# Kernel tuning notes

Hardware: AMD Instinct MI355X
Metric: run time of the kernel (lower is better)

Reference implementation:

```python
import jax, jax.numpy as jnp
import numpy as np
import math

D = 2048  # hidden_size
B, S = 4, 2048
EPS = 1e-5


def _ln(z, g, b):
    m = jnp.mean(z, axis=-1, keepdims=True)
    v = jnp.mean(jnp.square(z - m), axis=-1, keepdims=True)
    return (z - m) * jax.lax.rsqrt(v + EPS) * g + b


def _rotate_half(x):
    h = x.shape[-1] // 2
    return jnp.concatenate([-x[..., h:], x[..., :h]], axis=-1)


def _mas_normalize(logits):
    m = jnp.max(jnp.abs(logits), axis=-1, keepdims=True)
    return logits / (m + 1e-9)


def setup_inputs() -> dict:
    key = jax.random.key(0)
    ks = jax.random.split(key, 12)
    std = 0.02
    return {
        "x": jax.random.normal(ks[0], (B, S, D), dtype=jnp.float32),
        "position_ids": jnp.arange(S, dtype=jnp.int32),
        "ln1_g": jnp.ones((D,), jnp.float32),
        "ln1_b": jnp.zeros((D,), jnp.float32),
        # stacked params for [q, k, v, o]
        "mu_w": std * jax.random.normal(ks[1], (4, D, D), dtype=jnp.float32),
        "mu_b": jnp.zeros((4, D), jnp.float32),
        "proto_w": std * jax.random.normal(ks[2], (4, D, D), dtype=jnp.float32),
        "gate": jnp.zeros((4, D), jnp.float32),
        "pt_w": std * jax.random.normal(ks[3], (4, D, D), dtype=jnp.float32),
        "pln_g": jnp.ones((4, D), jnp.float32),
        "pln_b": jnp.zeros((4, D), jnp.float32),
        "incoming": std * jax.random.normal(ks[4], (4, D, D), dtype=jnp.float32),
    }


def reference(x, position_ids, ln1_g, ln1_b, mu_w, mu_b, proto_w, gate,
              pt_w, pln_g, pln_b, incoming):
    d = x.shape[-1]
    inv_sqrt_d = 1.0 / math.sqrt(d)

    # proto_state = proto_weight + LN(Linear(incoming))  per module [4, D, D]
    prc = jnp.einsum('nij,noj->nio', incoming, pt_w)
    proto_state = proto_w + _ln(prc, pln_g[:, None, :], pln_b[:, None, :])

    ln1_out = _ln(x, ln1_g, ln1_b)            # [B,S,D]
    ctx = jnp.mean(ln1_out, axis=1)           # [B,D]

    # qkv computation outputs: silu(ln1_out @ mu_w.T + mu_b) for n in {q,k,v}
    comp = jax.nn.silu(jnp.einsum('bsd,nod->nbso', ln1_out, mu_w[:3])
                       + mu_b[:3][:, None, None, :])            # [3,B,S,D]
    # routing from context vector
    match_ctx = jnp.einsum('bd,nod->nbo', ctx, proto_state[:3]) * inv_sqrt_d
    routing = match_ctx + gate[:3][:, None, :]                  # [3,B,D]
    gating = _mas_normalize(routing)
    masked = gating[:, :, None, :] * comp                       # [3,B,S,D]
    q, k, v = masked[0], masked[1], masked[2]

    # RoPE over full hidden dim (num_heads == 1)
    seq = position_ids.shape[0]
    inv_freq = 1.0 / (10000.0 ** (jnp.arange(0, d, 2, dtype=jnp.float32) / d))
    t = jnp.arange(seq, dtype=jnp.float32)
    freqs = t[:, None] * inv_freq[None, :]
    emb = jnp.concatenate([freqs, freqs], axis=-1)              # [S,D]
    cos = jnp.cos(emb)[position_ids]
    sin = jnp.sin(emb)[position_ids]
    q = q * cos + _rotate_half(q) * sin
    k = k * cos + _rotate_half(k) * sin

    # causal single-head attention, scale 1/sqrt(head_dim=D)
    scores = jnp.einsum('bqd,bkd->bqk', q, k) * inv_sqrt_d      # [B,S,S]
    causal = jnp.tril(jnp.ones((seq, seq), dtype=bool))
    scores = jnp.where(causal, scores, jnp.finfo(scores.dtype).min)
    probs = jax.nn.softmax(scores, axis=-1)
    attn_out = jnp.einsum('bqk,bkd->bqd', probs, v)             # [B,S,D]

    # output SPL + routing
    ctx_o = jnp.mean(attn_out, axis=1)
    c_o = jax.nn.silu(jnp.einsum('bsd,od->bso', attn_out, mu_w[3]) + mu_b[3])
    match_o = jnp.einsum('bd,od->bo', ctx_o, proto_state[3]) * inv_sqrt_d
    gating_o = _mas_normalize(match_o + gate[3])
    x_out = x + gating_o[:, None, :] * c_o
    return x_out
```

## Files before the change

### kernel.cpp

```cpp
#include <hip/hip_runtime.h>
#include <hip/hip_bf16.h>
#include <hip/hip_fp16.h>

#define Dh 2048
#define Bh 4
#define Sh 2048
#define NROW 8192
#define HALF 1024
#define INV_SQRT_D 0.022097086912079608f
#define LNEPS 1e-5f

typedef __hip_bfloat16 bf16;
typedef short short8 __attribute__((ext_vector_type(8)));
typedef float f32x4 __attribute__((ext_vector_type(4)));
typedef unsigned short ushort8v __attribute__((ext_vector_type(8)));
typedef unsigned short ushort4v __attribute__((ext_vector_type(4)));

__device__ inline float h2f_bits(unsigned short u) {
  __half h;
  *(unsigned short*)&h = u;
  return __half2float(h);
}

__device__ inline float warp_sum(float x) {
#pragma unroll
  for (int o = 32; o > 0; o >>= 1) x += __shfl_down(x, o);
  return x;
}
__device__ inline float warp_max(float x) {
#pragma unroll
  for (int o = 32; o > 0; o >>= 1) x = fmaxf(x, __shfl_down(x, o));
  return x;
}
__device__ inline float block_sum(float x, float* sm4) {
  x = warp_sum(x);
  int w = threadIdx.x >> 6;
  if ((threadIdx.x & 63) == 0) sm4[w] = x;
  __syncthreads();
  float r = sm4[0] + sm4[1] + sm4[2] + sm4[3];
  __syncthreads();
  return r;
}
__device__ inline float block_max(float x, float* sm4) {
  x = warp_max(x);
  int w = threadIdx.x >> 6;
  if ((threadIdx.x & 63) == 0) sm4[w] = x;
  __syncthreads();
  float r = fmaxf(fmaxf(sm4[0], sm4[1]), fmaxf(sm4[2], sm4[3]));
  __syncthreads();
  return r;
}

__device__ inline void gload_lds16(const void* g, void* lds) {
  __builtin_amdgcn_global_load_lds(
      (const __attribute__((address_space(1))) unsigned int*)(unsigned long long)g,
      (__attribute__((address_space(3))) unsigned int*)(unsigned long long)lds,
      16, 0, 0);
}

#define MM4(R, AF, B0, B1, B2, B3)                                             \
  acc[R][0] = __builtin_amdgcn_mfma_f32_16x16x32_bf16(AF, B0, acc[R][0], 0, 0, 0); \
  acc[R][1] = __builtin_amdgcn_mfma_f32_16x16x32_bf16(AF, B1, acc[R][1], 0, 0, 0); \
  acc[R][2] = __builtin_amdgcn_mfma_f32_16x16x32_bf16(AF, B2, acc[R][2], 0, 0, 0); \
  acc[R][3] = __builtin_amdgcn_mfma_f32_16x16x32_bf16(AF, B3, acc[R][3], 0, 0, 0);

template <int MODE>
__global__ __launch_bounds__(512) void pgemm(
    const bf16* __restrict__ Aall, const bf16* __restrict__ Ball,
    void* __restrict__ Call, int N, int K, int lda, int ldb,
    long sAz, long sBz, long sCz,
    const float* __restrict__ e0, const float* __restrict__ e1,
    const float* __restrict__ e2) {
  const int bm0 = blockIdx.x * 256;
  const int bn0 = blockIdx.y * 256;
  if (MODE == 2 && bn0 > bm0 + 255) return;
  const int z = blockIdx.z;
  const bf16* A = Aall + (long)z * sAz;
  const bf16* B = Ball + (long)z * sBz;

  __shared__ __align__(16) char smem[163840];
  const int tid = threadIdx.x;
  const int l = tid & 63, w = tid >> 6;
  const int wr = w >> 2, wc = w & 3;

  f32x4 acc[8][4] = {};
  const int nt = K >> 6;

  const int sg = (((l & 7) ^ ((l >> 3) & 7)) << 3);
  const int srow = (w << 3) + (l >> 3);
  const bf16* aS0 = A + (long)(bm0 + srow) * lda + sg;
  const bf16* aS1 = A + (long)(bm0 + 64 + srow) * lda + sg;
  const bf16* aS2 = A + (long)(bm0 + 128 + srow) * lda + sg;
  const bf16* aS3 = A + (long)(bm0 + 192 + srow) * lda + sg;
  const bf16* bT0 = B + (long)(bn0 + srow) * ldb + sg;
  const bf16* bT1 = B + (long)(bn0 + 64 + srow) * ldb + sg;
  const bf16* bT2 = B + (long)(bn0 + 128 + srow) * ldb + sg;
  const bf16* bT3 = B + (long)(bn0 + 192 + srow) * ldb + sg;
  char* const dA = smem + (w << 10);
  char* const dB = smem + 65536 + (w << 10);

  auto stageA = [&](int tt) {
    int boff = (tt & 1) << 15;
    gload_lds16(aS0 + (tt << 6), dA + boff);
    gload_lds16(aS1 + (tt << 6), dA + boff + 8192);
    gload_lds16(aS2 + (tt << 6), dA + boff + 16384);
    gload_lds16(aS3 + (tt << 6), dA + boff + 24576);
  };
  auto stageB = [&](int tt) {
    int boff = (tt % 3) << 15;
    gload_lds16(bT0 + (tt << 6), dB + boff);
    gload_lds16(bT1 + (tt << 6), dB + boff + 8192);
    gload_lds16(bT2 + (tt << 6), dB + boff + 16384);
    gload_lds16(bT3 + (tt << 6), dB + boff + 24576);
  };

  stageA(0); stageB(0);
  if (nt > 1) stageB(1);
  if (nt > 1) asm volatile("s_waitcnt vmcnt(4)" ::: "memory");
  else        asm volatile("s_waitcnt vmcnt(0)" ::: "memory");
  __builtin_amdgcn_sched_barrier(0);
  asm volatile("s_barrier" ::: "memory");

  const int rslot = (((l >> 4) ^ (l & 7)) << 4);
  const int abyte = (((wr << 7) + (l & 15)) << 7) + rslot;
  const int bbyte = (((wc << 6) + (l & 15)) << 7) + rslot;

  for (int t = 0; t < nt; ++t) {
    const char* Ab = smem + ((t & 1) << 15);
    const char* Bb = smem + 65536 + ((t % 3) << 15);
    short8 b00 = *(const short8*)(Bb + bbyte);
    short8 b01 = *(const short8*)(Bb + bbyte + 2048);
    short8 b02 = *(const short8*)(Bb + bbyte + 4096);
    short8 b03 = *(const short8*)(Bb + bbyte + 6144);
    short8 b10 = *(const short8*)(Bb + (bbyte ^ 64));
    short8 b11 = *(const short8*)(Bb + ((bbyte + 2048) ^ 64));
    short8 b12 = *(const short8*)(Bb + ((bbyte + 4096) ^ 64));
    short8 b13 = *(const short8*)(Bb + ((bbyte + 6144) ^ 64));
    short8 a0 = *(const short8*)(Ab + abyte);
    short8 a1 = *(const short8*)(Ab + abyte + 2048);
    short8 a2 = *(const short8*)(Ab + abyte + 4096);
    short8 a3 = *(const short8*)(Ab + abyte + 6144);
    short8 a4 = *(const short8*)(Ab + abyte + 8192);
    short8 a5 = *(const short8*)(Ab + abyte + 10240);
    short8 a6 = *(const short8*)(Ab + abyte + 12288);
    short8 a7 = *(const short8*)(Ab + abyte + 14336);
    if (t + 1 < nt) stageA(t + 1);
    MM4(0, a0, b00, b01, b02, b03) MM4(1, a1, b00, b01, b02, b03)
    MM4(2, a2, b00, b01, b02, b03) MM4(3, a3, b00, b01, b02, b03)
    MM4(4, a4, b00, b01, b02, b03) MM4(5, a5, b00, b01, b02, b03)
    MM4(6, a6, b00, b01, b02, b03) MM4(7, a7, b00, b01, b02, b03)
    short8 c0 = *(const short8*)(Ab + (abyte ^ 64));
    short8 c1 = *(const short8*)(Ab + ((abyte + 2048) ^ 64));
    short8 c2 = *(const short8*)(Ab + ((abyte + 4096) ^ 64));
    short8 c3 = *(const short8*)(Ab + ((abyte + 6144) ^ 64));
    short8 c4 = *(const short8*)(Ab + ((abyte + 8192) ^ 64));
    short8 c5 = *(const short8*)(Ab + ((abyte + 10240) ^ 64));
    short8 c6 = *(const short8*)(Ab + ((abyte + 12288) ^ 64));
    short8 c7 = *(const short8*)(Ab + ((abyte + 14336) ^ 64));
    if (t + 2 < nt) stageB(t + 2);
    MM4(0, c0, b10, b11, b12, b13) MM4(1, c1, b10, b11, b12, b13)
    MM4(2, c2, b10, b11, b12, b13) MM4(3, c3, b10, b11, b12, b13)
    MM4(4, c4, b10, b11, b12, b13) MM4(5, c5, b10, b11, b12, b13)
    MM4(6, c6, b10, b11, b12, b13) MM4(7, c7, b10, b11, b12, b13)
    if (t < nt - 1) {
      asm volatile("s_waitcnt lgkmcnt(0)" ::: "memory");
      if (t + 2 < nt) asm volatile("s_waitcnt vmcnt(4)" ::: "memory");
      else            asm volatile("s_waitcnt vmcnt(0)" ::: "memory");
      __builtin_amdgcn_sched_barrier(0);
      asm volatile("s_barrier" ::: "memory");
    }
  }

  const int lc = l & 15, lr4 = (l >> 4) << 2;
#pragma unroll
  for (int fr = 0; fr < 8; ++fr) {
    int gr0 = bm0 + (wr << 7) + fr * 16 + lr4;
#pragma unroll
    for (int fc = 0; fc < 4; ++fc) {
      int gc = bn0 + (wc << 6) + fc * 16 + lc;
#pragma unroll
      for (int qv = 0; qv < 4; ++qv) {
        int gr = gr0 + qv;
        float a = acc[fr][fc][qv];
        if (MODE == 0) {
          ((float*)Call + (long)z * sCz)[(long)gr * N + gc] = a;
        } else if (MODE == 1) {
          float val = a + e0[z * Dh + gc];
          float sil = val / (1.f + __expf(-val));
          int bb = gr >> 11;
          float g = e1[(z * Bh + bb) * Dh + gc];
          ((bf16*)Call + (long)z * sCz)[(long)gr * N + gc] =
              __float2bfloat16(sil * g);
        } else if (MODE == 2) {
          ((__half*)Call + (long)z * sCz)[(long)gr * N + gc] =
              __float2half(a * INV_SQRT_D);
        } else {
          float val = a + e0[gc];
          float sil = val / (1.f + __expf(-val));
          int bb = gr >> 11;
          ((float*)Call)[(long)gr * N + gc] =
              e2[(long)gr * N + gc] + e1[bb * Dh + gc] * sil;
        }
      }
    }
  }
}

#define MM(R, AF)                                                              \
  acc[R][0] = __builtin_amdgcn_mfma_f32_16x16x32_bf16(AF, b0, acc[R][0], 0, 0, 0); \
  acc[R][1] = __builtin_amdgcn_mfma_f32_16x16x32_bf16(AF, b1, acc[R][1], 0, 0, 0); \
  acc[R][2] = __builtin_amdgcn_mfma_f32_16x16x32_bf16(AF, b2, acc[R][2], 0, 0, 0); \
  acc[R][3] = __builtin_amdgcn_mfma_f32_16x16x32_bf16(AF, b3, acc[R][3], 0, 0, 0);

__global__ __launch_bounds__(512) void pgemm_h(
    const bf16* __restrict__ Aall, const bf16* __restrict__ Ball,
    bf16* __restrict__ Call, int N, int lda, int ldb,
    long sAz, long sBz, long sCz) {
  const int fid = blockIdx.x;
  const int p = fid >> 8, q = fid & 255;
  const int mh = q >> 5;
  const int z = (q >> 3) & 3, ni = q & 7;
  const int mi = p ? (15 - mh) : mh;
  const int bm0 = mi * 128, bn0 = ni * 256;
  const bf16* A = Aall + (long)z * sAz;
  const bf16* B = Ball + (long)z * sBz;

  __shared__ __align__(16) char smem[49152];
  const int tid = threadIdx.x;
  const int l = tid & 63, w = tid >> 6;
  const int wr = w >> 2, wc = w & 3;
  f32x4 acc[4][4] = {};
  const int nt = (bm0 + 128) >> 5;

  const int sg = (((l & 3) ^ ((l >> 3) & 3)) << 3);
  const int srow = (w << 4) + (l >> 2);
  const bf16* aS  = A + (long)(bm0 + srow) * lda + sg;
  const bf16* bS0 = B + (long)(bn0 + srow) * ldb + sg;
  const bf16* bS1 = B + (long)(bn0 + 128 + srow) * ldb + sg;
  char* const dA = smem + (w << 10);
  char* const dB = smem + 8192 + (w << 10);

  auto stageA = [&](int tt) {
    gload_lds16(aS + (tt << 5), dA + (tt & 1) * 24576);
  };
  auto stageB = [&](int tt) {
    int boff = (tt & 1) * 24576;
    gload_lds16(bS0 + (tt << 5), dB + boff);
    gload_lds16(bS1 + (tt << 5), dB + boff + 8192);
  };

  stageA(0); stageB(0);
  if (nt > 1) stageB(1);
  if (nt > 1) asm volatile("s_waitcnt vmcnt(2)" ::: "memory");
  else        asm volatile("s_waitcnt vmcnt(0)" ::: "memory");
  __builtin_amdgcn_sched_barrier(0);
  asm volatile("s_barrier" ::: "memory");

  const int rslot = (((l >> 4) ^ ((l >> 1) & 3)) << 4);
  const int abyte = (((wr << 6) + (l & 15)) << 6) + rslot;
  const int bbyte = (((wc << 6) + (l & 15)) << 6) + rslot;

  for (int t = 0; t < nt; ++t) {
    const char* Ab = smem + (t & 1) * 24576;
    const char* Bb = Ab + 8192;
    short8 b0 = *(const short8*)(Bb + bbyte);
    short8 b1 = *(const short8*)(Bb + bbyte + 1024);
    short8 b2 = *(const short8*)(Bb + bbyte + 2048);
    short8 b3 = *(const short8*)(Bb + bbyte + 3072);
    short8 a0 = *(const short8*)(Ab + abyte);
    short8 a1 = *(const short8*)(Ab + abyte + 1024);
    if (t + 1 < nt) stageA(t + 1);
    MM(0, a0) MM(1, a1)
    asm volatile("s_waitcnt lgkmcnt(0)" ::: "memory");
    asm volatile("s_barrier" ::: "memory");
    short8 a2 = *(const short8*)(Ab + abyte + 2048);
    short8 a3 = *(const short8*)(Ab + abyte + 3072);
    if (t + 2 < nt) stageB(t + 2);
    MM(2, a2) MM(3, a3)
    if (t < nt - 1) {
      asm volatile("s_waitcnt lgkmcnt(0)" ::: "memory");
      if (t + 2 < nt) asm volatile("s_waitcnt vmcnt(2)" ::: "memory");
      else            asm volatile("s_waitcnt vmcnt(0)" ::: "memory");
      __builtin_amdgcn_sched_barrier(0);
      asm volatile("s_barrier" ::: "memory");
    }
  }

  const int lc = l & 15, lr4 = (l >> 4) << 2;
  bf16* C = Call + (long)z * sCz;
#pragma unroll
  for (int fr = 0; fr < 4; ++fr) {
    int gr0 = bm0 + (wr << 6) + fr * 16 + lr4;
#pragma unroll
    for (int fc = 0; fc < 4; ++fc) {
      int gc = bn0 + (wc << 6) + fc * 16 + lc;
#pragma unroll
      for (int qv = 0; qv < 4; ++qv)
        C[(long)(gr0 + qv) * N + gc] = __float2bfloat16(acc[fr][fc][qv]);
    }
  }
}

__global__ __launch_bounds__(256) void cvt3_kernel(
    const float* __restrict__ s0, const float* __restrict__ s1,
    const float* __restrict__ s2, bf16* __restrict__ o0, bf16* __restrict__ o1,
    bf16* __restrict__ o2, long n) {
  const float* in = (blockIdx.y == 0) ? s0 : (blockIdx.y == 1) ? s1 : s2;
  bf16* out = (blockIdx.y == 0) ? o0 : (blockIdx.y == 1) ? o1 : o2;
  long i = ((long)blockIdx.x * 256 + threadIdx.x) * 4;
  if (i >= n) return;
  float4 v = *(const float4*)(in + i);
  out[i + 0] = __float2bfloat16(v.x);
  out[i + 1] = __float2bfloat16(v.y);
  out[i + 2] = __float2bfloat16(v.z);
  out[i + 3] = __float2bfloat16(v.w);
}

__global__ __launch_bounds__(256) void transpose_kernel(const bf16* __restrict__ in,
                                                        bf16* __restrict__ out) {
  __shared__ bf16 t[64][65];
  int b = blockIdx.z;
  int s0 = blockIdx.x * 64, d0 = blockIdx.y * 64;
  const bf16* ib = in + (long)b * Sh * Dh;
  bf16* ob = out + (long)b * Sh * Dh;
  int tx = threadIdx.x & 63, ty = threadIdx.x >> 6;
#pragma unroll
  for (int r = ty; r < 64; r += 4) t[r][tx] = ib[(long)(s0 + r) * Dh + d0 + tx];
  __syncthreads();
#pragma unroll
  for (int r = ty; r < 64; r += 4) ob[(long)(d0 + r) * Sh + s0 + tx] = t[tx][r];
}

__global__ __launch_bounds__(256) void ln1_kernel(const float* __restrict__ x,
    const float* __restrict__ g, const float* __restrict__ b, bf16* __restrict__ out) {
  __shared__ float sm4[4];
  long r = blockIdx.x;
  const float* row = x + r * Dh;
  int i0 = threadIdx.x * 4, i1 = 1024 + threadIdx.x * 4;
  float4 v0 = *(const float4*)(row + i0);
  float4 v1 = *(const float4*)(row + i1);
  float s = v0.x + v0.y + v0.z + v0.w + v1.x + v1.y + v1.z + v1.w;
  float s2 = v0.x * v0.x + v0.y * v0.y + v0.z * v0.z + v0.w * v0.w +
             v1.x * v1.x + v1.y * v1.y + v1.z * v1.z + v1.w * v1.w;
  s = block_sum(s, sm4);
  s2 = block_sum(s2, sm4);
  float mean = s * (1.f / Dh);
  float rstd = rsqrtf(s2 * (1.f / Dh) - mean * mean + LNEPS);
  float4 g0 = *(const float4*)(g + i0);
  float4 g1 = *(const float4*)(g + i1);
  float4 b0 = *(const float4*)(b + i0);
  float4 b1 = *(const float4*)(b + i1);
  ushort4v u0, u1;
  {
    bf16 t0 = __float2bfloat16((v0.x - mean) * rstd * g0.x + b0.x);
    bf16 t1 = __float2bfloat16((v0.y - mean) * rstd * g0.y + b0.y);
    bf16 t2 = __float2bfloat16((v0.z - mean) * rstd * g0.z + b0.z);
    bf16 t3 = __float2bfloat16((v0.w - mean) * rstd * g0.w + b0.w);
    u0[0] = *(unsigned short*)&t0; u0[1] = *(unsigned short*)&t1;
    u0[2] = *(unsigned short*)&t2; u0[3] = *(unsigned short*)&t3;
    bf16 s0b = __float2bfloat16((v1.x - mean) * rstd * g1.x + b1.x);
    bf16 s1b = __float2bfloat16((v1.y - mean) * rstd * g1.y + b1.y);
    bf16 s2b = __float2bfloat16((v1.z - mean) * rstd * g1.z + b1.z);
    bf16 s3b = __float2bfloat16((v1.w - mean) * rstd * g1.w + b1.w);
    u1[0] = *(unsigned short*)&s0b; u1[1] = *(unsigned short*)&s1b;
    u1[2] = *(unsigned short*)&s2b; u1[3] = *(unsigned short*)&s3b;
  }
  *(ushort4v*)(out + r * Dh + i0) = u0;
  *(ushort4v*)(out + r * Dh + i1) = u1;
}

__global__ __launch_bounds__(256) void meanrow_kernel(const bf16* __restrict__ in,
                                                      float* __restrict__ outbd) {
  int gid = blockIdx.x * 256 + threadIdx.x;
  int s0 = blockIdx.y * 128;
  long base = ((long)(gid >> 11) * Sh + s0) * Dh + (gid & 2047);
  float s = 0.f;
  for (int t = 0; t < 128; ++t) s += __bfloat162float(in[base + (long)t * Dh]);
  atomicAdd(&outbd[gid], s * (1.f / Sh));
}

__global__ __launch_bounds__(256) void route_kernel(
    const float* __restrict__ prc, const float* __restrict__ proto_w,
    const float* __restrict__ pln_g, const float* __restrict__ pln_b,
    const float* __restrict__ gate, const float* __restrict__ ctx,
    float* __restrict__ routing, float* __restrict__ ps3) {
  __shared__ float sm4[4];
  int i = blockIdx.x, n = blockIdx.y;
  long rb = ((long)n * Dh + i) * Dh;
  float v[8];
  float s = 0.f, s2 = 0.f;
#pragma unroll
  for (int c = 0; c < 8; ++c) {
    float t = prc[rb + threadIdx.x + c * 256];
    v[c] = t; s += t; s2 += t * t;
  }
  s = block_sum(s, sm4);
  s2 = block_sum(s2, sm4);
  float mean = s * (1.f / Dh);
  float rstd = rsqrtf(s2 * (1.f / Dh) - mean * mean + LNEPS);
  if (n == 3) {
#pragma unroll
    for (int c = 0; c < 8; ++c) {
      int o = threadIdx.x + c * 256;
      float ps = proto_w[rb + o] + (v[c] - mean) * rstd * pln_g[3 * Dh + o] + pln_b[3 * Dh + o];
      ps3[(long)i * Dh + o] = ps;
    }
  } else {
    float acc[4] = {0.f, 0.f, 0.f, 0.f};
#pragma unroll
    for (int c = 0; c < 8; ++c) {
      int o = threadIdx.x + c * 256;
      float ps = proto_w[rb + o] + (v[c] - mean) * rstd * pln_g[n * Dh + o] + pln_b[n * Dh + o];
#pragma unroll
      for (int b = 0; b < 4; ++b) acc[b] += ps * ctx[b * Dh + o];
    }
    for (int b = 0; b < 4; ++b) {
      float r = block_sum(acc[b], sm4);
      if (threadIdx.x == 0)
        routing[(n * 4 + b) * Dh + i] = r * INV_SQRT_D + gate[n * Dh + i];
    }
  }
}

__global__ __launch_bounds__(256) void route_o_kernel(
    const float* __restrict__ ps3, const float* __restrict__ ctxo,
    const float* __restrict__ gate, float* __restrict__ routing) {
  __shared__ float sm4[4];
  int i = blockIdx.x;
  float acc[4] = {0.f, 0.f, 0.f, 0.f};
#pragma unroll
  for (int c = 0; c < 8; ++c) {
    int o = threadIdx.x + c * 256;
    float p = ps3[(long)i * Dh + o];
#pragma unroll
    for (int b = 0; b < 4; ++b) acc[b] += p * ctxo[b * Dh + o];
  }
  for (int b = 0; b < 4; ++b) {
    float r = block_sum(acc[b], sm4);
    if (threadIdx.x == 0)
      routing[(12 + b) * Dh + i] = r * INV_SQRT_D + gate[3 * Dh + i];
  }
}

__global__ __launch_bounds__(256) void masnorm_kernel(const float* __restrict__ rin,
                                                      float* __restrict__ gout) {
  __shared__ float sm4[4];
  long r = blockIdx.x;
  float m = 0.f;
#pragma unroll
  for (int c = 0; c < 8; ++c)
    m = fmaxf(m, fabsf(rin[r * Dh + threadIdx.x + c * 256]));
  m = block_max(m, sm4);
  float inv = 1.f / (m + 1e-9f);
#pragma unroll
  for (int c = 0; c < 8; ++c) {
    int o = threadIdx.x + c * 256;
    gout[r * Dh + o] = rin[r * Dh + o] * inv;
  }
}

__global__ __launch_bounds__(256) void rope_table_kernel(float* __restrict__ cosT,
                                                         float* __restrict__ sinT) {
  int idx = blockIdx.x * 256 + threadIdx.x;
  int t = idx >> 10, f = idx & 1023;
  float inv_freq = expf(-(float)f * (9.210340371976184f / 1024.f));
  float ang = (float)t * inv_freq;
  cosT[idx] = cosf(ang);
  sinT[idx] = sinf(ang);
}

__global__ __launch_bounds__(256) void rope_kernel(bf16* __restrict__ q, bf16* __restrict__ k,
    const int* __restrict__ pos, const float* __restrict__ cosT,
    const float* __restrict__ sinT) {
  long r = blockIdx.x;
  int s = (int)(r & (Sh - 1));
  int p = pos[s];
#pragma unroll
  for (int c = 0; c < 4; ++c) {
    int t = threadIdx.x + c * 256;
    float cv = cosT[(long)p * HALF + t];
    float sv = sinT[(long)p * HALF + t];
    long i1 = r * Dh + t, i2 = i1 + HALF;
    float q1 = __bfloat162float(q[i1]), q2 = __bfloat162float(q[i2]);
    q[i1] = __float2bfloat16(q1 * cv - q2 * sv);
    q[i2] = __float2bfloat16(q2 * cv + q1 * sv);
    float k1 = __bfloat162float(k[i1]), k2 = __bfloat162float(k[i2]);
    k[i1] = __float2bfloat16(k1 * cv - k2 * sv);
    k[i2] = __float2bfloat16(k2 * cv + k1 * sv);
  }
}

__global__ __launch_bounds__(256) void softmax_kernel(const unsigned short* __restrict__ scores,
                                                      bf16* __restrict__ probs) {
  __shared__ float buf[Sh];
  __shared__ float sm4[4];
  long r = blockIdx.x;
  int qi = (int)(r & (Sh - 1));
  const unsigned short* row = scores + r * (long)Sh;
  bf16* prow = probs + r * (long)Sh;
  int tid = threadIdx.x;
  int n = qi + 1, nv = n & ~7;
  float m = -3.0e38f;
  for (int o = tid * 8; o < nv; o += 2048) {
    ushort8v v = *(const ushort8v*)(row + o);
#pragma unroll
    for (int j = 0; j < 8; ++j) {
      float x = h2f_bits(v[j]);
      buf[o + j] = x;
      m = fmaxf(m, x);
    }
  }
  for (int o = nv + tid; o < n; o += 256) {
    float x = h2f_bits(row[o]); buf[o] = x; m = fmaxf(m, x);
  }
  m = block_max(m, sm4);
  float s = 0.f;
  for (int o = tid; o < n; o += 256) {
    float e = __expf(buf[o] - m); buf[o] = e; s += e;
  }
  s = block_sum(s, sm4);
  float inv = 1.f / s;
  for (int o = tid * 8; o < nv; o += 2048) {
    ushort8v u;
#pragma unroll
    for (int j = 0; j < 8; ++j) {
      bf16 t = __float2bfloat16(buf[o + j] * inv);
      u[j] = *(unsigned short*)&t;
    }
    *(ushort8v*)(prow + o) = u;
  }
  for (int o = nv + tid; o < n; o += 256) prow[o] = __float2bfloat16(buf[o] * inv);
  int za = (n + 7) & ~7;
  for (int o = n + tid; o < za && o < Sh; o += 256) prow[o] = __float2bfloat16(0.f);
  ushort8v zz = {0, 0, 0, 0, 0, 0, 0, 0};
  for (int o = za + tid * 8; o < Sh; o += 2048) *(ushort8v*)(prow + o) = zz;
}

extern "C" void kernel_launch(void* const* d_in, const int* in_sizes, int n_in,
                              void* d_out, int out_size, void* d_ws, size_t ws_size,
                              hipStream_t stream) {
  const float* x       = (const float*)d_in[0];
  const int*   pos     = (const int*)d_in[1];
  const float* ln1_g   = (const float*)d_in[2];
  const float* ln1_b   = (const float*)d_in[3];
  const float* mu_w    = (const float*)d_in[4];
  const float* mu_b    = (const float*)d_in[5];
  const float* proto_w = (const float*)d_in[6];
  const float* gate    = (const float*)d_in[7];
  const float* pt_w    = (const float*)d_in[8];
  const float* pln_g   = (const float*)d_in[9];
  const float* pln_b   = (const float*)d_in[10];
  const float* incoming= (const float*)d_in[11];

  char* w = (char*)d_ws;
  const long BF = 33554432L;
  bf16*  ln1    = (bf16*)(w);
  bf16*  qb     = (bf16*)(w + BF);
  bf16*  kb     = (bf16*)(w + 2 * BF);
  bf16*  vb     = (bf16*)(w + 3 * BF);
  bf16*  attn   = (bf16*)(w + 4 * BF);
  bf16*  mu_wb  = (bf16*)(w + 5 * BF);
  bf16*  ptw_b  = (bf16*)(w + 6 * BF);
  bf16*  vT     = ptw_b;
  bf16*  inc_b  = (bf16*)(w + 7 * BF);
  bf16*  probs  = inc_b;
  float* ps3    = (float*)(w + 8 * BF);
  float* cosT   = (float*)(w + 8 * BF + 16777216L);
  float* sinT   = cosT + (long)Sh * HALF;
  float* ctx    = sinT + (long)Sh * HALF;
  float* ctxo   = ctx + Bh * Dh;
  float* routing= ctxo + Bh * Dh;
  float* gating = routing + 16 * Dh;
  float*  prc    = (float*)d_out;
  __half* scores = (__half*)d_out;

  const long DD4 = 4L * Dh * Dh;

  hipMemsetAsync(ctx, 0, 2L * Bh * Dh * sizeof(float), stream);

  rope_table_kernel<<<(Sh * HALF) / 256, 256, 0, stream>>>(cosT, sinT);
  cvt3_kernel<<<dim3(DD4 / 1024, 3), 256, 0, stream>>>(
      mu_w, incoming, pt_w, mu_wb, inc_b, ptw_b, DD4);
  ln1_kernel<<<NROW, 256, 0, stream>>>(x, ln1_g, ln1_b, ln1);
  meanrow_kernel<<<dim3(32, 16), 256, 0, stream>>>(ln1, ctx);
  pgemm<0><<<dim3(8, 8, 4), 512, 0, stream>>>(
      inc_b, ptw_b, prc, Dh, Dh, Dh, Dh,
      (long)Dh * Dh, (long)Dh * Dh, (long)Dh * Dh, nullptr, nullptr, nullptr);
  route_kernel<<<dim3(Dh, 4), 256, 0, stream>>>(prc, proto_w, pln_g, pln_b,
                                                gate, ctx, routing, ps3);
  masnorm_kernel<<<12, 256, 0, stream>>>(routing, gating);
  pgemm<1><<<dim3(32, 8, 3), 512, 0, stream>>>(
      ln1, mu_wb, qb, Dh, Dh, Dh, Dh,
      0L, (long)Dh * Dh, (long)NROW * Dh, mu_b, gating, nullptr);
  rope_kernel<<<NROW, 256, 0, stream>>>(qb, kb, pos, cosT, sinT);
  pgemm<2><<<dim3(8, 8, 4), 512, 0, stream>>>(
      qb, kb, scores, Sh, Dh, Dh, Dh,
      (long)Sh * Dh, (long)Sh * Dh, (long)Sh * Sh, nullptr, nullptr, nullptr);
  softmax_kernel<<<Bh * Sh, 256, 0, stream>>>((const unsigned short*)scores, probs);
  transpose_kernel<<<dim3(32, 32, 4), 256, 0, stream>>>(vb, vT);
  pgemm_h<<<512, 512, 0, stream>>>(
      probs, vT, attn, Dh, Sh, Sh,
      (long)Sh * Sh, (long)Dh * Sh, (long)Sh * Dh);
  meanrow_kernel<<<dim3(32, 16), 256, 0, stream>>>(attn, ctxo);
  route_o_kernel<<<Dh, 256, 0, stream>>>(ps3, ctxo, gate, routing);
  masnorm_kernel<<<4, 256, 0, stream>>>(routing + 12 * Dh, gating + 12 * Dh);
  pgemm<4><<<dim3(32, 8, 1), 512, 0, stream>>>(
      attn, mu_wb + 3L * Dh * Dh, d_out, Dh, Dh, Dh, Dh,
      0L, 0L, 0L, mu_b + 3 * Dh, gating + 12 * Dh, x);
}
```

Before: 625.5 us.

## Deepen K tile to 64 and triple-buffer B in pgemm_h

Doubles the per-iteration K depth of the pgemm_h MFMA loop from 32 to 64, double-buffering A and triple-buffering B in a 128KB LDS area with a wider XOR swizzle. This removes the mid-iteration barrier and halves the number of loop iterations and barriers. The aim is to cut synchronisation overhead and give global loads more time to land. In exchange, the much larger LDS footprint lets fewer blocks fit per CU, which reduces latency hiding from occupancy.

After: 625.6 us. No clear change (+0.0%).

```diff
diff --git a/kernel.cpp b/kernel.cpp
--- a/kernel.cpp
+++ b/kernel.cpp
@@ -206,12 +206,6 @@
   }
 }
 
-#define MM(R, AF)                                                              \
-  acc[R][0] = __builtin_amdgcn_mfma_f32_16x16x32_bf16(AF, b0, acc[R][0], 0, 0, 0); \
-  acc[R][1] = __builtin_amdgcn_mfma_f32_16x16x32_bf16(AF, b1, acc[R][1], 0, 0, 0); \
-  acc[R][2] = __builtin_amdgcn_mfma_f32_16x16x32_bf16(AF, b2, acc[R][2], 0, 0, 0); \
-  acc[R][3] = __builtin_amdgcn_mfma_f32_16x16x32_bf16(AF, b3, acc[R][3], 0, 0, 0);
-
 __global__ __launch_bounds__(512) void pgemm_h(
     const bf16* __restrict__ Aall, const bf16* __restrict__ Ball,
     bf16* __restrict__ Call, int N, int lda, int ldb,
@@ -225,61 +219,74 @@
   const bf16* A = Aall + (long)z * sAz;
   const bf16* B = Ball + (long)z * sBz;
 
-  __shared__ __align__(16) char smem[49152];
+  __shared__ __align__(16) char smem[131072];
   const int tid = threadIdx.x;
   const int l = tid & 63, w = tid >> 6;
   const int wr = w >> 2, wc = w & 3;
   f32x4 acc[4][4] = {};
-  const int nt = (bm0 + 128) >> 5;
-
-  const int sg = (((l & 3) ^ ((l >> 3) & 3)) << 3);
-  const int srow = (w << 4) + (l >> 2);
-  const bf16* aS  = A + (long)(bm0 + srow) * lda + sg;
-  const bf16* bS0 = B + (long)(bn0 + srow) * ldb + sg;
-  const bf16* bS1 = B + (long)(bn0 + 128 + srow) * ldb + sg;
+  const int nt = (bm0 + 128) >> 6;
+
+  const int sg = (((l & 7) ^ ((l >> 3) & 7)) << 3);
+  const int srow = (w << 3) + (l >> 3);
+  const bf16* aS0 = A + (long)(bm0 + srow) * lda + sg;
+  const bf16* aS1 = A + (long)(bm0 + 64 + srow) * lda + sg;
+  const bf16* bT0 = B + (long)(bn0 + srow) * ldb + sg;
+  const bf16* bT1 = B + (long)(bn0 + 64 + srow) * ldb + sg;
+  const bf16* bT2 = B + (long)(bn0 + 128 + srow) * ldb + sg;
+  const bf16* bT3 = B + (long)(bn0 + 192 + srow) * ldb + sg;
   char* const dA = smem + (w << 10);
-  char* const dB = smem + 8192 + (w << 10);
+  char* const dB = smem + 32768 + (w << 10);
 
   auto stageA = [&](int tt) {
-    gload_lds16(aS + (tt << 5), dA + (tt & 1) * 24576);
+    int boff = (tt & 1) << 14;
+    gload_lds16(aS0 + (tt << 6), dA + boff);
+    gload_lds16(aS1 + (tt << 6), dA + boff + 8192);
   };
   auto stageB = [&](int tt) {
-    int boff = (tt & 1) * 24576;
-    gload_lds16(bS0 + (tt << 5), dB + boff);
-    gload_lds16(bS1 + (tt << 5), dB + boff + 8192);
+    int boff = (tt % 3) << 15;
+    gload_lds16(bT0 + (tt << 6), dB + boff);
+    gload_lds16(bT1 + (tt << 6), dB + boff + 8192);
+    gload_lds16(bT2 + (tt << 6), dB + boff + 16384);
+    gload_lds16(bT3 + (tt << 6), dB + boff + 24576);
   };
 
-  stageA(0); stageB(0);
-  if (nt > 1) stageB(1);
-  if (nt > 1) asm volatile("s_waitcnt vmcnt(2)" ::: "memory");
-  else        asm volatile("s_waitcnt vmcnt(0)" ::: "memory");
+  stageA(0); stageB(0); stageB(1);
+  asm volatile("s_waitcnt vmcnt(4)" ::: "memory");
   __builtin_amdgcn_sched_barrier(0);
   asm volatile("s_barrier" ::: "memory");
 
-  const int rslot = (((l >> 4) ^ ((l >> 1) & 3)) << 4);
-  const int abyte = (((wr << 6) + (l & 15)) << 6) + rslot;
-  const int bbyte = (((wc << 6) + (l & 15)) << 6) + rslot;
+  const int rslot = (((l >> 4) ^ (l & 7)) << 4);
+  const int abyte = (((wr << 6) + (l & 15)) << 7) + rslot;
+  const int bbyte = (((wc << 6) + (l & 15)) << 7) + rslot;
 
   for (int t = 0; t < nt; ++t) {
-    const char* Ab = smem + (t & 1) * 24576;
-    const char* Bb = Ab + 8192;
-    short8 b0 = *(const short8*)(Bb + bbyte);
-    short8 b1 = *(const short8*)(Bb + bbyte + 1024);
-    short8 b2 = *(const short8*)(Bb + bbyte + 2048);
-    short8 b3 = *(const short8*)(Bb + bbyte + 3072);
+    const char* Ab = smem + ((t & 1) << 14);
+    const char* Bb = smem + 32768 + ((t % 3) << 15);
+    short8 b00 = *(const short8*)(Bb + bbyte);
+    short8 b01 = *(const short8*)(Bb + bbyte + 2048);
+    short8 b02 = *(const short8*)(Bb + bbyte + 4096);
+    short8 b03 = *(const short8*)(Bb + bbyte + 6144);
+    short8 b10 = *(const short8*)(Bb + (bbyte ^ 64));
+    short8 b11 = *(const short8*)(Bb + ((bbyte + 2048) ^ 64));
+    short8 b12 = *(const short8*)(Bb + ((bbyte + 4096) ^ 64));
+    short8 b13 = *(const short8*)(Bb + ((bbyte + 6144) ^ 64));
     short8 a0 = *(const short8*)(Ab + abyte);
-    short8 a1 = *(const short8*)(Ab + abyte + 1024);
+    short8 a1 = *(const short8*)(Ab + abyte + 2048);
+    short8 a2 = *(const short8*)(Ab + abyte + 4096);
+    short8 a3 = *(const short8*)(Ab + abyte + 6144);
     if (t + 1 < nt) stageA(t + 1);
-    MM(0, a0) MM(1, a1)
-    asm volatile("s_waitcnt lgkmcnt(0)" ::: "memory");
-    asm volatile("s_barrier" ::: "memory");
-    short8 a2 = *(const short8*)(Ab + abyte + 2048);
-    short8 a3 = *(const short8*)(Ab + abyte + 3072);
+    MM4(0, a0, b00, b01, b02, b03) MM4(1, a1, b00, b01, b02, b03)
+    MM4(2, a2, b00, b01, b02, b03) MM4(3, a3, b00, b01, b02, b03)
+    short8 c0 = *(const short8*)(Ab + (abyte ^ 64));
+    short8 c1 = *(const short8*)(Ab + ((abyte + 2048) ^ 64));
+    short8 c2 = *(const short8*)(Ab + ((abyte + 4096) ^ 64));
+    short8 c3 = *(const short8*)(Ab + ((abyte + 6144) ^ 64));
     if (t + 2 < nt) stageB(t + 2);
-    MM(2, a2) MM(3, a3)
+    MM4(0, c0, b10, b11, b12, b13) MM4(1, c1, b10, b11, b12, b13)
+    MM4(2, c2, b10, b11, b12, b13) MM4(3, c3, b10, b11, b12, b13)
     if (t < nt - 1) {
       asm volatile("s_waitcnt lgkmcnt(0)" ::: "memory");
-      if (t + 2 < nt) asm volatile("s_waitcnt vmcnt(2)" ::: "memory");
+      if (t + 2 < nt) asm volatile("s_waitcnt vmcnt(4)" ::: "memory");
       else            asm volatile("s_waitcnt vmcnt(0)" ::: "memory");
       __builtin_amdgcn_sched_barrier(0);
       asm volatile("s_barrier" ::: "memory");
```
